# Performance work log

Measured on AMD Instinct MI355X. Metric: run time of the kernel, lower is better.

The kernel has to match this reference:

```python
import jax, jax.numpy as jnp
import numpy as np

K = 64
M = 256
V = 5000

def setup_inputs() -> dict:
    key = jax.random.key(0)
    ks = jax.random.split(key, 8)
    feat_x = jax.random.normal(ks[0], (1, V, M), dtype=jnp.float32)
    feat_y = jax.random.normal(ks[1], (1, V, M), dtype=jnp.float32)
    evals_x = jnp.sort(jax.random.uniform(ks[2], (1, K), dtype=jnp.float32))
    evals_y = jnp.sort(jax.random.uniform(ks[3], (1, K), dtype=jnp.float32))
    evecs_trans_x = jax.random.normal(ks[4], (1, K, V), dtype=jnp.float32) / np.sqrt(V)
    evecs_trans_y = jax.random.normal(ks[5], (1, K, V), dtype=jnp.float32) / np.sqrt(V)
    eye = jnp.eye(K, dtype=jnp.float32)
    sqrtMk_x = (eye + 0.05 * jax.random.normal(ks[6], (K, K), dtype=jnp.float32))[None]
    sqrtMk_y = (eye + 0.05 * jax.random.normal(ks[7], (K, K), dtype=jnp.float32))[None]
    return {"feat_x": feat_x, "feat_y": feat_y, "evals_x": evals_x, "evals_y": evals_y,
            "evecs_trans_x": evecs_trans_x, "evecs_trans_y": evecs_trans_y,
            "sqrtMk_x": sqrtMk_x, "sqrtMk_y": sqrtMk_y}

LMBDA = 0.001

def _fmap(fx, fy, ex, ey, tx, ty, sx, sy):
    # squeeze batch dim of 1 (as in torch .squeeze())
    fx, fy = fx[0], fy[0]            # [V, m]
    ex, ey = ex[0], ey[0]            # [k]
    tx, ty = tx[0], ty[0]            # [k, V]
    sx, sy = sx[0], sy[0]            # [k, k]
    A = tx @ fx                      # [k, m] spectral coeffs of feat_x
    B = sy @ (ty @ fy)               # adapt_feature=True: premultiply by sqrtMk_y
    k, m = A.shape
    vec_B = B.T.reshape(m * k, 1)
    At_Ik = jnp.kron(A.T, sy)        # [m*k, k*k] (adapt_feature -> Ik = sqrtMk_y)
    first = At_Ik.T @ At_Ik          # [k^2, k^2]
    # adapt_mask=True branch
    inv_sx = jnp.linalg.inv(sx)
    lx = jnp.diag(ex)
    ly = jnp.diag(ey)
    lx_Ik = jnp.kron(lx @ inv_sx, sy)
    Ik_ly = jnp.kron(inv_sx, sy @ ly)
    Delta = lx_Ik - Ik_ly
    second = Delta.T @ Delta
    rhs = At_Ik.T @ vec_B
    op = first + LMBDA * second
    C = jnp.linalg.solve(op, rhs)
    return C.reshape(k, k).T[None]   # [1, k, k]

def reference(feat_x, feat_y, evals_x, evals_y, evecs_trans_x, evecs_trans_y, sqrtMk_x, sqrtMk_y):
    # bidirectional=False -> only Cxy (Cyx is None in the torch module)
    return _fmap(feat_x, feat_y, evals_x, evals_y, evecs_trans_x, evecs_trans_y, sqrtMk_x, sqrtMk_y)
```

## Files before the change

### kernel.cpp

```cpp
#include <hip/hip_runtime.h>

#define LMBDA 0.001f
#define NS_SY 4
#define NS_G  5
#define NS_SX 5
#define OUTER 3
#define LDP 68

#define WS_A    0
#define WS_FY   16384
#define WS_G1   32768
#define WS_T1   36864
#define WS_R2   40960
#define WS_R4   45056
#define WS_GINV 49152
#define WS_C    53248
#define WS_FYAT 57344

#define FMA4(ar, xs, b) { ar[0]=fmaf((xs),(b).x,ar[0]); ar[1]=fmaf((xs),(b).y,ar[1]); \
                          ar[2]=fmaf((xs),(b).z,ar[2]); ar[3]=fmaf((xs),(b).w,ar[3]); }

template<int SA, int SB>
__device__ __forceinline__ void mm64(const float* __restrict__ A,
                                     const float* __restrict__ B,
                                     int ti, int tj, float a[4][4]) {
    #pragma unroll 4
    for (int k = 0; k < 64; k += 4) {
        float4 av0 = *(const float4*)&A[(4 * ti + 0) * SA + k];
        float4 av1 = *(const float4*)&A[(4 * ti + 1) * SA + k];
        float4 av2 = *(const float4*)&A[(4 * ti + 2) * SA + k];
        float4 av3 = *(const float4*)&A[(4 * ti + 3) * SA + k];
        float4 b0 = *(const float4*)&B[(k + 0) * SB + 4 * tj];
        float4 b1 = *(const float4*)&B[(k + 1) * SB + 4 * tj];
        float4 b2 = *(const float4*)&B[(k + 2) * SB + 4 * tj];
        float4 b3 = *(const float4*)&B[(k + 3) * SB + 4 * tj];
        FMA4(a[0], av0.x, b0); FMA4(a[0], av0.y, b1); FMA4(a[0], av0.z, b2); FMA4(a[0], av0.w, b3);
        FMA4(a[1], av1.x, b0); FMA4(a[1], av1.y, b1); FMA4(a[1], av1.z, b2); FMA4(a[1], av1.w, b3);
        FMA4(a[2], av2.x, b0); FMA4(a[2], av2.y, b1); FMA4(a[2], av2.z, b2); FMA4(a[2], av2.w, b3);
        FMA4(a[3], av3.x, b0); FMA4(a[3], av3.y, b1); FMA4(a[3], av3.z, b2); FMA4(a[3], av3.w, b3);
    }
}

__global__ __launch_bounds__(256) void k1_gemm(
    const float* __restrict__ tx, const float* __restrict__ fx,
    const float* __restrict__ ty, const float* __restrict__ fy,
    float* __restrict__ wsA, float* __restrict__ wsFy)
{
    __shared__ float sT[64 * LDP];
    __shared__ float sF[64 * LDP];
    const int tid = threadIdx.x;
    const int ti = tid >> 4, tj = tid & 15;
    const int mat = blockIdx.x >> 2;
    const int m0 = (blockIdx.x & 3) << 6;
    const float* __restrict__ T = mat ? ty : tx;
    const float* __restrict__ F = mat ? fy : fx;
    float* __restrict__ Out = mat ? wsFy : wsA;

    float acc[4][4];
    #pragma unroll
    for (int r = 0; r < 4; ++r)
        #pragma unroll
        for (int c = 0; c < 4; ++c) acc[r][c] = 0.f;

    for (int sc = blockIdx.y; sc * 64 < 5000; sc += 27) {
        const int v0 = sc << 6;
        int vlen = 5000 - v0; if (vlen > 64) vlen = 64;
        #pragma unroll
        for (int w = 0; w < 4; ++w) {
            const int fidx = tid + (w << 8);
            const int row = fidx >> 4, q = fidx & 15;
            const int vv = q << 2;
            if (vv < vlen) {
                float4 val = *(const float4*)(T + (size_t)row * 5000 + v0 + vv);
                sT[(vv + 0) * LDP + row] = val.x;
                sT[(vv + 1) * LDP + row] = val.y;
                sT[(vv + 2) * LDP + row] = val.z;
                sT[(vv + 3) * LDP + row] = val.w;
            }
            if (row < vlen) {
                *(float4*)&sF[row * LDP + (q << 2)] =
                    *(const float4*)(F + (size_t)(v0 + row) * 256 + m0 + (q << 2));
            }
        }
        __syncthreads();
        for (int v = 0; v < vlen; ++v) {
            float4 av = *(const float4*)&sT[v * LDP + 4 * ti];
            float4 bv = *(const float4*)&sF[v * LDP + 4 * tj];
            FMA4(acc[0], av.x, bv); FMA4(acc[1], av.y, bv);
            FMA4(acc[2], av.z, bv); FMA4(acc[3], av.w, bv);
        }
        __syncthreads();
    }
    #pragma unroll
    for (int r = 0; r < 4; ++r)
        #pragma unroll
        for (int c = 0; c < 4; ++c)
            atomicAdd(&Out[(4 * ti + r) * 256 + m0 + 4 * tj + c], acc[r][c]);
}

__device__ __forceinline__ void ns_invert(float* sM, float* sX, float* sY,
                                          int iters, int ti, int tj,
                                          int tid, float alpha)
{
    for (int idx = tid; idx < 4096; idx += 256) {
        int i = idx >> 6, j = idx & 63;
        sX[i * LDP + j] = (i == j) ? alpha : 0.f;
    }
    __syncthreads();
    for (int it = 0; it < iters; ++it) {
        float y[4][4];
        #pragma unroll
        for (int r = 0; r < 4; ++r)
            #pragma unroll
            for (int c = 0; c < 4; ++c) y[r][c] = 0.f;
        mm64<LDP, LDP>(sM, sX, ti, tj, y);
        #pragma unroll
        for (int r = 0; r < 4; ++r) {
            float4 v = {y[r][0], y[r][1], y[r][2], y[r][3]};
            *(float4*)&sY[(4 * ti + r) * 64 + 4 * tj] = v;
        }
        __syncthreads();
        float z[4][4];
        #pragma unroll
        for (int r = 0; r < 4; ++r)
            #pragma unroll
            for (int c = 0; c < 4; ++c) z[r][c] = 0.f;
        mm64<LDP, 64>(sX, sY, ti, tj, z);
        __syncthreads();
        #pragma unroll
        for (int r = 0; r < 4; ++r) {
            float4 xv = *(const float4*)&sX[(4 * ti + r) * LDP + 4 * tj];
            xv.x = 2.f * xv.x - z[r][0];
            xv.y = 2.f * xv.y - z[r][1];
            xv.z = 2.f * xv.z - z[r][2];
            xv.w = 2.f * xv.w - z[r][3];
            *(float4*)&sX[(4 * ti + r) * LDP + 4 * tj] = xv;
        }
        __syncthreads();
    }
}

__global__ __launch_bounds__(256, 1) void k2_prep(
    const float* __restrict__ wsA, const float* __restrict__ wsFy,
    const float* __restrict__ sx, const float* __restrict__ sy,
    const float* __restrict__ ex, const float* __restrict__ ey,
    float* __restrict__ ws)
{
    extern __shared__ __align__(16) float lds2[];
    const int tid = threadIdx.x;
    const int ti = tid >> 4, tj = tid & 15;
    const int b = blockIdx.x;

    if (b == 0) {
        float* sSy = lds2;
        float* sXx = lds2 + 4352;
        float* sYy = lds2 + 8704;
        float* sH  = lds2 + 12800;
        float* sV  = lds2 + 16896;
        for (int idx = tid; idx < 1024; idx += 256) {
            int i = idx >> 4, j4 = (idx & 15) << 2;
            *(float4*)&sSy[i * LDP + j4] = *(const float4*)&sy[i * 64 + j4];
        }
        if (tid < 64) sV[tid] = ey[tid];
        __syncthreads();
        {
            float h[4][4];
            #pragma unroll
            for (int r = 0; r < 4; ++r)
                #pragma unroll
                for (int c = 0; c < 4; ++c) h[r][c] = 0.f;
            for (int k = 0; k < 64; ++k) {
                float4 av = *(const float4*)&sSy[k * LDP + 4 * ti];
                float4 bv = *(const float4*)&sSy[k * LDP + 4 * tj];
                FMA4(h[0], av.x, bv); FMA4(h[1], av.y, bv);
                FMA4(h[2], av.z, bv); FMA4(h[3], av.w, bv);
            }
            #pragma unroll
            for (int r = 0; r < 4; ++r) {
                float4 v = {h[r][0], h[r][1], h[r][2], h[r][3]};
                *(float4*)&sH[(4 * ti + r) * 64 + 4 * tj] = v;
            }
        }
        __syncthreads();
        ns_invert(sSy, sXx, sYy, NS_SY, ti, tj, tid, 1.0f);
        {
            float h[4][4];
            #pragma unroll
            for (int r = 0; r < 4; ++r)
                #pragma unroll
                for (int c = 0; c < 4; ++c) h[r][c] = 0.f;
            for (int m = 0; m < 64; m += 4) {
                float4 av[4], bv[4];
                #pragma unroll
                for (int r = 0; r < 4; ++r) av[r] = *(const float4*)&sXx[(4 * ti + r) * LDP + m];
                #pragma unroll
                for (int c = 0; c < 4; ++c) bv[c] = *(const float4*)&sXx[(4 * tj + c) * LDP + m];
                #pragma unroll
                for (int r = 0; r < 4; ++r)
                    #pragma unroll
                    for (int c = 0; c < 4; ++c)
                        h[r][c] += av[r].x * bv[c].x + av[r].y * bv[c].y
                                 + av[r].z * bv[c].z + av[r].w * bv[c].w;
            }
            __syncthreads();
            #pragma unroll
            for (int r = 0; r < 4; ++r) {
                float4 v = {h[r][0], h[r][1], h[r][2], h[r][3]};
                *(float4*)&sSy[(4 * ti + r) * LDP + 4 * tj] = v;
            }
        }
        __syncthreads();
        {
            float a[4][4];
            #pragma unroll
            for (int r = 0; r < 4; ++r)
                #pragma unroll
                for (int c = 0; c < 4; ++c) a[r][c] = 0.f;
            #pragma unroll 4
            for (int k = 0; k < 64; k += 4) {
                float4 av[4];
                #pragma unroll
                for (int r = 0; r < 4; ++r) av[r] = *(const float4*)&sSy[(4 * ti + r) * LDP + k];
                #pragma unroll
                for (int q = 0; q < 4; ++q) {
                    float e = sV[k + q];
                    float4 bv = *(const float4*)&sH[(k + q) * 64 + 4 * tj];
                    bv.x *= e; bv.y *= e; bv.z *= e; bv.w *= e;
                    float xq[4] = {av[0].x, av[1].x, av[2].x, av[3].x};
                    if (q == 1) { xq[0]=av[0].y; xq[1]=av[1].y; xq[2]=av[2].y; xq[3]=av[3].y; }
                    if (q == 2) { xq[0]=av[0].z; xq[1]=av[1].z; xq[2]=av[2].z; xq[3]=av[3].z; }
                    if (q == 3) { xq[0]=av[0].w; xq[1]=av[1].w; xq[2]=av[2].w; xq[3]=av[3].w; }
                    #pragma unroll
                    for (int r = 0; r < 4; ++r) FMA4(a[r], xq[r], bv);
                }
            }
            #pragma unroll
            for (int r = 0; r < 4; ++r) {
                float4 v = {a[r][0], a[r][1], a[r][2], a[r][3]};
                *(float4*)&ws[WS_C + (4 * ti + r) * 64 + 4 * tj] = v;
            }
        }
    } else if (b == 1) {
        float* sA = lds2;
        float* sG = lds2 + 4352;
        float* sX = lds2 + 8704;
        float* sY = lds2 + 13056;
        float* sV = lds2 + 17152;
        float a[4][4];
        #pragma unroll
        for (int r = 0; r < 4; ++r)
            #pragma unroll
            for (int c = 0; c < 4; ++c) a[r][c] = 0.f;
        for (int ch = 0; ch < 4; ++ch) {
            for (int idx = tid; idx < 1024; idx += 256) {
                int i = idx >> 4, m4 = (idx & 15) << 2;
                *(float4*)&sA[i * LDP + m4] =
                    *(const float4*)&wsA[i * 256 + (ch << 6) + m4];
            }
            __syncthreads();
            for (int m = 0; m < 64; m += 4) {
                float4 av[4], bv[4];
                #pragma unroll
                for (int r = 0; r < 4; ++r) av[r] = *(const float4*)&sA[(4 * ti + r) * LDP + m];
                #pragma unroll
                for (int c = 0; c < 4; ++c) bv[c] = *(const float4*)&sA[(4 * tj + c) * LDP + m];
                #pragma unroll
                for (int r = 0; r < 4; ++r)
                    #pragma unroll
                    for (int c = 0; c < 4; ++c)
                        a[r][c] += av[r].x * bv[c].x + av[r].y * bv[c].y
                                 + av[r].z * bv[c].z + av[r].w * bv[c].w;
            }
            __syncthreads();
        }
        #pragma unroll
        for (int r = 0; r < 4; ++r) {
            float4 v = {a[r][0], a[r][1], a[r][2], a[r][3]};
            *(float4*)&sG[(4 * ti + r) * LDP + 4 * tj] = v;
            *(float4*)&ws[WS_G1 + (4 * ti + r) * 64 + 4 * tj] = v;
        }
        __syncthreads();
        if (tid < 64) {
            float s = 0.f;
            for (int j4 = 0; j4 < 64; j4 += 4) {
                float4 v = *(const float4*)&sG[tid * LDP + j4];
                s += v.x * v.x + v.y * v.y + v.z * v.z + v.w * v.w;
            }
            sV[tid] = s;
            sV[64 + tid] = sG[tid * LDP + tid];
        }
        __syncthreads();
        float f2 = 0.f, tr = 0.f;
        for (int i = 0; i < 64; ++i) { f2 += sV[i]; tr += sV[64 + i]; }
        ns_invert(sG, sX, sY, NS_G, ti, tj, tid, tr / f2);
        for (int idx = tid; idx < 1024; idx += 256) {
            int i = idx >> 4, j4 = (idx & 15) << 2;
            *(float4*)&ws[WS_GINV + i * 64 + j4] = *(const float4*)&sX[i * LDP + j4];
        }
    } else if (b == 2) {
        float* sM = lds2;
        float* sX = lds2 + 4352;
        float* sY = lds2 + 8704;
        float* sV = lds2 + 12800;
        for (int idx = tid; idx < 1024; idx += 256) {
            int i = idx >> 4, j4 = (idx & 15) << 2;
            *(float4*)&sM[i * LDP + j4] = *(const float4*)&sx[i * 64 + j4];
        }
        if (tid < 64) sV[tid] = ex[tid];
        __syncthreads();
        ns_invert(sM, sX, sY, NS_SX, ti, tj, tid, 1.0f);
        float aR2[4][4], aR4[4][4], aT1[4][4];
        #pragma unroll
        for (int r = 0; r < 4; ++r)
            #pragma unroll
            for (int c = 0; c < 4; ++c) { aR2[r][c] = 0.f; aR4[r][c] = 0.f; aT1[r][c] = 0.f; }
        for (int k = 0; k < 64; ++k) {
            float e = sV[k], e2 = e * e;
            float4 av = *(const float4*)&sX[k * LDP + 4 * ti];
            float4 bv = *(const float4*)&sX[k * LDP + 4 * tj];
            float avv[4] = {av.x, av.y, av.z, av.w};
            #pragma unroll
            for (int r = 0; r < 4; ++r) {
                FMA4(aR4[r], avv[r], bv);
                float ea = e * avv[r];
                FMA4(aR2[r], ea, bv);
                float e2a = e2 * avv[r];
                FMA4(aT1[r], e2a, bv);
            }
        }
        #pragma unroll
        for (int r = 0; r < 4; ++r) {
            int o = (4 * ti + r) * 64 + 4 * tj;
            float4 v2 = {aR2[r][0], aR2[r][1], aR2[r][2], aR2[r][3]};
            float4 v4 = {aR4[r][0], aR4[r][1], aR4[r][2], aR4[r][3]};
            float4 v1 = {aT1[r][0], aT1[r][1], aT1[r][2], aT1[r][3]};
            *(float4*)&ws[WS_R2 + o] = v2;
            *(float4*)&ws[WS_R4 + o] = v4;
            *(float4*)&ws[WS_T1 + o] = v1;
        }
    } else {
        float* sFy = lds2;
        float* sAx = lds2 + 4352;
        float a[4][4];
        #pragma unroll
        for (int r = 0; r < 4; ++r)
            #pragma unroll
            for (int c = 0; c < 4; ++c) a[r][c] = 0.f;
        for (int ch = 0; ch < 4; ++ch) {
            for (int idx = tid; idx < 1024; idx += 256) {
                int i = idx >> 4, m4 = (idx & 15) << 2;
                *(float4*)&sFy[i * LDP + m4] = *(const float4*)&wsFy[i * 256 + (ch << 6) + m4];
                *(float4*)&sAx[i * LDP + m4] = *(const float4*)&wsA[i * 256 + (ch << 6) + m4];
            }
            __syncthreads();
            for (int m = 0; m < 64; m += 4) {
                float4 av[4], bv[4];
                #pragma unroll
                for (int r = 0; r < 4; ++r) av[r] = *(const float4*)&sFy[(4 * ti + r) * LDP + m];
                #pragma unroll
                for (int c = 0; c < 4; ++c) bv[c] = *(const float4*)&sAx[(4 * tj + c) * LDP + m];
                #pragma unroll
                for (int r = 0; r < 4; ++r)
                    #pragma unroll
                    for (int c = 0; c < 4; ++c)
                        a[r][c] += av[r].x * bv[c].x + av[r].y * bv[c].y
                                 + av[r].z * bv[c].z + av[r].w * bv[c].w;
            }
            __syncthreads();
        }
        #pragma unroll
        for (int r = 0; r < 4; ++r) {
            float4 v = {a[r][0], a[r][1], a[r][2], a[r][3]};
            *(float4*)&ws[WS_FYAT + (4 * ti + r) * 64 + 4 * tj] = v;
        }
    }
}

__global__ __launch_bounds__(256, 1) void k3_solve(
    const float* __restrict__ ws, const float* __restrict__ ey_g,
    float* __restrict__ out)
{
    extern __shared__ __align__(16) float lds3[];
    float* cM1   = lds3;
    float* cR2   = lds3 + 4096;
    float* cR4   = lds3 + 8192;
    float* cGinv = lds3 + 12288;
    float* sE    = lds3 + 16384;
    float* sX    = lds3 + 20480;
    float* cC    = lds3 + 24832;
    float* sW    = lds3 + 29184;
    const int tid = threadIdx.x;
    const int ti = tid >> 4, tj = tid & 15;

    for (int idx = tid; idx < 1024; idx += 256) {
        int i = idx >> 4, j4 = (idx & 15) << 2;
        int o = i * 64 + j4;
        float4 g = *(const float4*)&ws[WS_G1 + o];
        float4 t = *(const float4*)&ws[WS_T1 + o];
        float4 m = {fmaf(LMBDA, t.x, g.x), fmaf(LMBDA, t.y, g.y),
                    fmaf(LMBDA, t.z, g.z), fmaf(LMBDA, t.w, g.w)};
        *(float4*)&cM1[o]   = m;
        *(float4*)&cR2[o]   = *(const float4*)&ws[WS_R2 + o];
        *(float4*)&cR4[o]   = *(const float4*)&ws[WS_R4 + o];
        *(float4*)&cGinv[o] = *(const float4*)&ws[WS_GINV + o];
        *(float4*)&cC[i * LDP + j4] = *(const float4*)&ws[WS_C + o];
    }
    float4 eyv = *(const float4*)&ey_g[4 * ti];
    float eyr[4] = {eyv.x, eyv.y, eyv.z, eyv.w};
    float leyr[4];
    #pragma unroll
    for (int r = 0; r < 4; ++r) leyr[r] = LMBDA * eyr[r];

    float fyr[4][4], xreg[4][4];
    #pragma unroll
    for (int r = 0; r < 4; ++r) {
        float4 v = *(const float4*)&ws[WS_FYAT + (4 * ti + r) * 64 + 4 * tj];
        fyr[r][0] = v.x; fyr[r][1] = v.y; fyr[r][2] = v.z; fyr[r][3] = v.w;
        float4 z = {0.f, 0.f, 0.f, 0.f};
        *(float4*)&sX[(4 * ti + r) * LDP + 4 * tj] = z;
        #pragma unroll
        for (int c = 0; c < 4; ++c) xreg[r][c] = 0.f;
    }
    __syncthreads();

    float E1[4][4];
    for (int it = 0; it < OUTER; ++it) {
        {
            float Sm[4][4], S2[4][4], S4[4][4];
            #pragma unroll
            for (int r = 0; r < 4; ++r)
                #pragma unroll
                for (int c = 0; c < 4; ++c) { Sm[r][c] = 0.f; S2[r][c] = 0.f; S4[r][c] = 0.f; }
            #pragma unroll 2
            for (int k = 0; k < 64; k += 4) {
                float4 av[4];
                #pragma unroll
                for (int r = 0; r < 4; ++r)
                    av[r] = *(const float4*)&sX[(4 * ti + r) * LDP + k];
                #pragma unroll
                for (int q = 0; q < 4; ++q) {
                    float4 mv = *(const float4*)&cM1[(k + q) * 64 + 4 * tj];
                    float4 qv = *(const float4*)&cR2[(k + q) * 64 + 4 * tj];
                    float4 rv = *(const float4*)&cR4[(k + q) * 64 + 4 * tj];
                    float xq[4] = {av[0].x, av[1].x, av[2].x, av[3].x};
                    if (q == 1) { xq[0]=av[0].y; xq[1]=av[1].y; xq[2]=av[2].y; xq[3]=av[3].y; }
                    if (q == 2) { xq[0]=av[0].z; xq[1]=av[1].z; xq[2]=av[2].z; xq[3]=av[3].z; }
                    if (q == 3) { xq[0]=av[0].w; xq[1]=av[1].w; xq[2]=av[2].w; xq[3]=av[3].w; }
                    #pragma unroll
                    for (int r = 0; r < 4; ++r) {
                        FMA4(Sm[r], xq[r], mv);
                        FMA4(S2[r], xq[r], qv);
                        FMA4(S4[r], xq[r], rv);
                    }
                }
            }
            #pragma unroll
            for (int r = 0; r < 4; ++r) {
                float4 e2;
                e2.x = LMBDA * fmaf(eyr[r], S4[r][0], -S2[r][0]);
                e2.y = LMBDA * fmaf(eyr[r], S4[r][1], -S2[r][1]);
                e2.z = LMBDA * fmaf(eyr[r], S4[r][2], -S2[r][2]);
                e2.w = LMBDA * fmaf(eyr[r], S4[r][3], -S2[r][3]);
                *(float4*)&sE[(4 * ti + r) * 64 + 4 * tj] = e2;
                #pragma unroll
                for (int c = 0; c < 4; ++c)
                    E1[r][c] = fmaf(-leyr[r], S2[r][c], Sm[r][c]);
            }
        }
        __syncthreads();
        {
            float Z[4][4];
            #pragma unroll
            for (int r = 0; r < 4; ++r)
                #pragma unroll
                for (int c = 0; c < 4; ++c) Z[r][c] = 0.f;
            mm64<LDP, 64>(cC, sE, ti, tj, Z);
            #pragma unroll
            for (int r = 0; r < 4; ++r) {
                float4 w;
                w.x = fyr[r][0] - E1[r][0] - Z[r][0];
                w.y = fyr[r][1] - E1[r][1] - Z[r][1];
                w.z = fyr[r][2] - E1[r][2] - Z[r][2];
                w.w = fyr[r][3] - E1[r][3] - Z[r][3];
                *(float4*)&sW[(4 * ti + r) * LDP + 4 * tj] = w;
            }
        }
        __syncthreads();
        {
            float dX[4][4];
            #pragma unroll
            for (int r = 0; r < 4; ++r)
                #pragma unroll
                for (int c = 0; c < 4; ++c) dX[r][c] = 0.f;
            mm64<LDP, 64>(sW, cGinv, ti, tj, dX);
            #pragma unroll
            for (int r = 0; r < 4; ++r) {
                float4 v;
                #pragma unroll
                for (int c = 0; c < 4; ++c) xreg[r][c] += dX[r][c];
                v.x = xreg[r][0]; v.y = xreg[r][1]; v.z = xreg[r][2]; v.w = xreg[r][3];
                *(float4*)&sX[(4 * ti + r) * LDP + 4 * tj] = v;
                if (it == OUTER - 1)
                    *(float4*)&out[(4 * ti + r) * 64 + 4 * tj] = v;
            }
        }
        if (it == OUTER - 1) break;
        __syncthreads();
    }
}

extern "C" void kernel_launch(void* const* d_in, const int* in_sizes, int n_in,
                              void* d_out, int out_size, void* d_ws, size_t ws_size,
                              hipStream_t stream) {
    (void)in_sizes; (void)n_in; (void)out_size; (void)ws_size;
    const float* fx = (const float*)d_in[0];
    const float* fy = (const float*)d_in[1];
    const float* ex = (const float*)d_in[2];
    const float* ey = (const float*)d_in[3];
    const float* tx = (const float*)d_in[4];
    const float* ty = (const float*)d_in[5];
    const float* sx = (const float*)d_in[6];
    const float* sy = (const float*)d_in[7];
    float* ws = (float*)d_ws;
    float* out = (float*)d_out;

    (void)hipFuncSetAttribute((const void*)k2_prep,
                              hipFuncAttributeMaxDynamicSharedMemorySize, 69120);
    (void)hipFuncSetAttribute((const void*)k3_solve,
                              hipFuncAttributeMaxDynamicSharedMemorySize, 134144);

    (void)hipMemsetAsync(d_ws, 0, 2 * 64 * 256 * sizeof(float), stream);
    k1_gemm<<<dim3(8, 27), 256, 0, stream>>>(tx, fx, ty, fy, ws + WS_A, ws + WS_FY);
    k2_prep<<<4, 256, 69120, stream>>>(ws + WS_A, ws + WS_FY, sx, sy, ex, ey, ws);
    k3_solve<<<1, 256, 134144, stream>>>(ws, ey, out);
}
```

Measured before the change: 181.5 us.

## Fuse prep and solve kernels with atomic-counter sync and split-K partial buffers

Merges the prep and solve kernels into one launch where helper blocks signal completion through a global atomic counter. When the workspace is large enough, the spectral GEMM writes per-split partial sums, which removes the memset and the atomics and cuts the split count. It also drops one Newton-Schulz iteration for inv(sx) and restructures some small matmuls. In exchange the design relies on blocks of one launch running concurrently (spin-wait) and accepts a slightly less converged inverse.

```diff
diff --git a/kernel.cpp b/kernel.cpp
--- a/kernel.cpp
+++ b/kernel.cpp
@@ -3,19 +3,19 @@
 #define LMBDA 0.001f
 #define NS_SY 4
 #define NS_G  5
-#define NS_SX 5
+#define NS_SX 4
 #define OUTER 3
 #define LDP 68
-
-#define WS_A    0
-#define WS_FY   16384
-#define WS_G1   32768
-#define WS_T1   36864
-#define WS_R2   40960
-#define WS_R4   45056
-#define WS_GINV 49152
-#define WS_C    53248
-#define WS_FYAT 57344
+#define SPLITS 8
+
+#define WS_R2   32768
+#define WS_R4   36864
+#define WS_T1   40960
+#define WS_C    45056
+#define WS_FYAT 49152
+#define WS_CTR  53248
+#define WS_PART 53312
+#define WS_NEED ((WS_PART + SPLITS * 32768) * 4)
 
 #define FMA4(ar, xs, b) { ar[0]=fmaf((xs),(b).x,ar[0]); ar[1]=fmaf((xs),(b).y,ar[1]); \
                           ar[2]=fmaf((xs),(b).z,ar[2]); ar[3]=fmaf((xs),(b).w,ar[3]); }
@@ -41,63 +41,6 @@
     }
 }
 
-__global__ __launch_bounds__(256) void k1_gemm(
-    const float* __restrict__ tx, const float* __restrict__ fx,
-    const float* __restrict__ ty, const float* __restrict__ fy,
-    float* __restrict__ wsA, float* __restrict__ wsFy)
-{
-    __shared__ float sT[64 * LDP];
-    __shared__ float sF[64 * LDP];
-    const int tid = threadIdx.x;
-    const int ti = tid >> 4, tj = tid & 15;
-    const int mat = blockIdx.x >> 2;
-    const int m0 = (blockIdx.x & 3) << 6;
-    const float* __restrict__ T = mat ? ty : tx;
-    const float* __restrict__ F = mat ? fy : fx;
-    float* __restrict__ Out = mat ? wsFy : wsA;
-
-    float acc[4][4];
-    #pragma unroll
-    for (int r = 0; r < 4; ++r)
-        #pragma unroll
-        for (int c = 0; c < 4; ++c) acc[r][c] = 0.f;
-
-    for (int sc = blockIdx.y; sc * 64 < 5000; sc += 27) {
-        const int v0 = sc << 6;
-        int vlen = 5000 - v0; if (vlen > 64) vlen = 64;
-        #pragma unroll
-        for (int w = 0; w < 4; ++w) {
-            const int fidx = tid + (w << 8);
-            const int row = fidx >> 4, q = fidx & 15;
-            const int vv = q << 2;
-            if (vv < vlen) {
-                float4 val = *(const float4*)(T + (size_t)row * 5000 + v0 + vv);
-                sT[(vv + 0) * LDP + row] = val.x;
-                sT[(vv + 1) * LDP + row] = val.y;
-                sT[(vv + 2) * LDP + row] = val.z;
-                sT[(vv + 3) * LDP + row] = val.w;
-            }
-            if (row < vlen) {
-                *(float4*)&sF[row * LDP + (q << 2)] =
-                    *(const float4*)(F + (size_t)(v0 + row) * 256 + m0 + (q << 2));
-            }
-        }
-        __syncthreads();
-        for (int v = 0; v < vlen; ++v) {
-            float4 av = *(const float4*)&sT[v * LDP + 4 * ti];
-            float4 bv = *(const float4*)&sF[v * LDP + 4 * tj];
-            FMA4(acc[0], av.x, bv); FMA4(acc[1], av.y, bv);
-            FMA4(acc[2], av.z, bv); FMA4(acc[3], av.w, bv);
-        }
-        __syncthreads();
-    }
-    #pragma unroll
-    for (int r = 0; r < 4; ++r)
-        #pragma unroll
-        for (int c = 0; c < 4; ++c)
-            atomicAdd(&Out[(4 * ti + r) * 256 + m0 + 4 * tj + c], acc[r][c]);
-}
-
 __device__ __forceinline__ void ns_invert(float* sM, float* sX, float* sY,
                                           int iters, int ti, int tj,
                                           int tid, float alpha)
@@ -140,26 +83,96 @@
     }
 }
 
-__global__ __launch_bounds__(256, 1) void k2_prep(
-    const float* __restrict__ wsA, const float* __restrict__ wsFy,
+__global__ __launch_bounds__(256) void k1_gemm(
+    const float* __restrict__ tx, const float* __restrict__ fx,
+    const float* __restrict__ ty, const float* __restrict__ fy,
+    float* __restrict__ ws, int nparts, int pbase)
+{
+    __shared__ float sT[64 * LDP];
+    __shared__ float sF[64 * LDP];
+    const int tid = threadIdx.x;
+    const int ti = tid >> 4, tj = tid & 15;
+    const int mat = blockIdx.x >> 2;
+    const int m0 = (blockIdx.x & 3) << 6;
+    const float* __restrict__ T = mat ? ty : tx;
+    const float* __restrict__ F = mat ? fy : fx;
+    float* __restrict__ Out = ws + pbase +
+        (nparts > 1 ? (int)blockIdx.y * 32768 : 0) + mat * 16384;
+
+    if (blockIdx.x == 0 && blockIdx.y == 0 && tid == 0)
+        ((unsigned*)(ws + WS_CTR))[0] = 0u;
+
+    float acc[4][4];
+    #pragma unroll
+    for (int r = 0; r < 4; ++r)
+        #pragma unroll
+        for (int c = 0; c < 4; ++c) acc[r][c] = 0.f;
+
+    for (int sc = blockIdx.y; sc * 64 < 5000; sc += gridDim.y) {
+        const int v0 = sc << 6;
+        int vlen = 5000 - v0; if (vlen > 64) vlen = 64;
+        #pragma unroll
+        for (int w = 0; w < 4; ++w) {
+            const int fidx = tid + (w << 8);
+            const int row = fidx >> 4, q = fidx & 15;
+            const int vv = q << 2;
+            if (vv < vlen) {
+                float4 val = *(const float4*)(T + (size_t)row * 5000 + v0 + vv);
+                sT[(vv + 0) * LDP + row] = val.x;
+                sT[(vv + 1) * LDP + row] = val.y;
+                sT[(vv + 2) * LDP + row] = val.z;
+                sT[(vv + 3) * LDP + row] = val.w;
+            }
+            if (row < vlen) {
+                *(float4*)&sF[row * LDP + (q << 2)] =
+                    *(const float4*)(F + (size_t)(v0 + row) * 256 + m0 + (q << 2));
+            }
+        }
+        __syncthreads();
+        for (int v = 0; v < vlen; ++v) {
+            float4 av = *(const float4*)&sT[v * LDP + 4 * ti];
+            float4 bv = *(const float4*)&sF[v * LDP + 4 * tj];
+            FMA4(acc[0], av.x, bv); FMA4(acc[1], av.y, bv);
+            FMA4(acc[2], av.z, bv); FMA4(acc[3], av.w, bv);
+        }
+        __syncthreads();
+    }
+    if (nparts > 1) {
+        #pragma unroll
+        for (int r = 0; r < 4; ++r) {
+            float4 v = {acc[r][0], acc[r][1], acc[r][2], acc[r][3]};
+            *(float4*)&Out[(4 * ti + r) * 256 + m0 + 4 * tj] = v;
+        }
+    } else {
+        #pragma unroll
+        for (int r = 0; r < 4; ++r)
+            #pragma unroll
+            for (int c = 0; c < 4; ++c)
+                atomicAdd(&Out[(4 * ti + r) * 256 + m0 + 4 * tj + c], acc[r][c]);
+    }
+}
+
+__global__ __launch_bounds__(256, 1) void k23_fused(
+    float* __restrict__ ws,
     const float* __restrict__ sx, const float* __restrict__ sy,
     const float* __restrict__ ex, const float* __restrict__ ey,
-    float* __restrict__ ws)
+    float* __restrict__ out, int nparts, int pbase)
 {
-    extern __shared__ __align__(16) float lds2[];
+    extern __shared__ __align__(16) float lds[];
     const int tid = threadIdx.x;
     const int ti = tid >> 4, tj = tid & 15;
     const int b = blockIdx.x;
-
-    if (b == 0) {
-        float* sSy = lds2;
-        float* sXx = lds2 + 4352;
-        float* sYy = lds2 + 8704;
-        float* sH  = lds2 + 12800;
-        float* sV  = lds2 + 16896;
+    unsigned* ctr = (unsigned*)(ws + WS_CTR);
+
+    if (b == 1) {
+        float* s0 = lds;
+        float* s1 = lds + 4352;
+        float* s2 = lds + 8704;
+        float* s3 = lds + 12800;
+        float* sV = lds + 16896;
         for (int idx = tid; idx < 1024; idx += 256) {
             int i = idx >> 4, j4 = (idx & 15) << 2;
-            *(float4*)&sSy[i * LDP + j4] = *(const float4*)&sy[i * 64 + j4];
+            *(float4*)&s0[i * LDP + j4] = *(const float4*)&sy[i * 64 + j4];
         }
         if (tid < 64) sV[tid] = ey[tid];
         __syncthreads();
@@ -170,43 +183,42 @@
                 #pragma unroll
                 for (int c = 0; c < 4; ++c) h[r][c] = 0.f;
             for (int k = 0; k < 64; ++k) {
-                float4 av = *(const float4*)&sSy[k * LDP + 4 * ti];
-                float4 bv = *(const float4*)&sSy[k * LDP + 4 * tj];
+                float4 av = *(const float4*)&s0[k * LDP + 4 * ti];
+                float4 bv = *(const float4*)&s0[k * LDP + 4 * tj];
                 FMA4(h[0], av.x, bv); FMA4(h[1], av.y, bv);
                 FMA4(h[2], av.z, bv); FMA4(h[3], av.w, bv);
             }
             #pragma unroll
             for (int r = 0; r < 4; ++r) {
                 float4 v = {h[r][0], h[r][1], h[r][2], h[r][3]};
-                *(float4*)&sH[(4 * ti + r) * 64 + 4 * tj] = v;
-            }
-        }
-        __syncthreads();
-        ns_invert(sSy, sXx, sYy, NS_SY, ti, tj, tid, 1.0f);
+                *(float4*)&s3[(4 * ti + r) * 64 + 4 * tj] = v;
+            }
+        }
+        __syncthreads();
+        ns_invert(s0, s1, s2, NS_SY, ti, tj, tid, 1.0f);
         {
-            float h[4][4];
+            float z[4][4];
             #pragma unroll
             for (int r = 0; r < 4; ++r)
                 #pragma unroll
-                for (int c = 0; c < 4; ++c) h[r][c] = 0.f;
-            for (int m = 0; m < 64; m += 4) {
-                float4 av[4], bv[4];
-                #pragma unroll
-                for (int r = 0; r < 4; ++r) av[r] = *(const float4*)&sXx[(4 * ti + r) * LDP + m];
-                #pragma unroll
-                for (int c = 0; c < 4; ++c) bv[c] = *(const float4*)&sXx[(4 * tj + c) * LDP + m];
-                #pragma unroll
-                for (int r = 0; r < 4; ++r)
-                    #pragma unroll
-                    for (int c = 0; c < 4; ++c)
-                        h[r][c] += av[r].x * bv[c].x + av[r].y * bv[c].y
-                                 + av[r].z * bv[c].z + av[r].w * bv[c].w;
+                for (int c = 0; c < 4; ++c) z[r][c] = 0.f;
+            #pragma unroll 4
+            for (int k = 0; k < 64; ++k) {
+                float e = sV[k];
+                float a0 = s1[k * LDP + 4 * ti + 0];
+                float a1 = s1[k * LDP + 4 * ti + 1];
+                float a2 = s1[k * LDP + 4 * ti + 2];
+                float a3 = s1[k * LDP + 4 * ti + 3];
+                float4 bv = *(const float4*)&s3[k * 64 + 4 * tj];
+                bv.x *= e; bv.y *= e; bv.z *= e; bv.w *= e;
+                FMA4(z[0], a0, bv); FMA4(z[1], a1, bv);
+                FMA4(z[2], a2, bv); FMA4(z[3], a3, bv);
             }
             __syncthreads();
             #pragma unroll
             for (int r = 0; r < 4; ++r) {
-                float4 v = {h[r][0], h[r][1], h[r][2], h[r][3]};
-                *(float4*)&sSy[(4 * ti + r) * LDP + 4 * tj] = v;
+                float4 v = {z[r][0], z[r][1], z[r][2], z[r][3]};
+                *(float4*)&s2[(4 * ti + r) * 64 + 4 * tj] = v;
             }
         }
         __syncthreads();
@@ -216,99 +228,28 @@
             for (int r = 0; r < 4; ++r)
                 #pragma unroll
                 for (int c = 0; c < 4; ++c) a[r][c] = 0.f;
-            #pragma unroll 4
-            for (int k = 0; k < 64; k += 4) {
-                float4 av[4];
-                #pragma unroll
-                for (int r = 0; r < 4; ++r) av[r] = *(const float4*)&sSy[(4 * ti + r) * LDP + k];
-                #pragma unroll
-                for (int q = 0; q < 4; ++q) {
-                    float e = sV[k + q];
-                    float4 bv = *(const float4*)&sH[(k + q) * 64 + 4 * tj];
-                    bv.x *= e; bv.y *= e; bv.z *= e; bv.w *= e;
-                    float xq[4] = {av[0].x, av[1].x, av[2].x, av[3].x};
-                    if (q == 1) { xq[0]=av[0].y; xq[1]=av[1].y; xq[2]=av[2].y; xq[3]=av[3].y; }
-                    if (q == 2) { xq[0]=av[0].z; xq[1]=av[1].z; xq[2]=av[2].z; xq[3]=av[3].z; }
-                    if (q == 3) { xq[0]=av[0].w; xq[1]=av[1].w; xq[2]=av[2].w; xq[3]=av[3].w; }
-                    #pragma unroll
-                    for (int r = 0; r < 4; ++r) FMA4(a[r], xq[r], bv);
-                }
-            }
+            mm64<LDP, 64>(s1, s2, ti, tj, a);
             #pragma unroll
             for (int r = 0; r < 4; ++r) {
                 float4 v = {a[r][0], a[r][1], a[r][2], a[r][3]};
                 *(float4*)&ws[WS_C + (4 * ti + r) * 64 + 4 * tj] = v;
             }
         }
-    } else if (b == 1) {
-        float* sA = lds2;
-        float* sG = lds2 + 4352;
-        float* sX = lds2 + 8704;
-        float* sY = lds2 + 13056;
-        float* sV = lds2 + 17152;
-        float a[4][4];
-        #pragma unroll
-        for (int r = 0; r < 4; ++r)
-            #pragma unroll
-            for (int c = 0; c < 4; ++c) a[r][c] = 0.f;
-        for (int ch = 0; ch < 4; ++ch) {
-            for (int idx = tid; idx < 1024; idx += 256) {
-                int i = idx >> 4, m4 = (idx & 15) << 2;
-                *(float4*)&sA[i * LDP + m4] =
-                    *(const float4*)&wsA[i * 256 + (ch << 6) + m4];
-            }
-            __syncthreads();
-            for (int m = 0; m < 64; m += 4) {
-                float4 av[4], bv[4];
-                #pragma unroll
-                for (int r = 0; r < 4; ++r) av[r] = *(const float4*)&sA[(4 * ti + r) * LDP + m];
-                #pragma unroll
-                for (int c = 0; c < 4; ++c) bv[c] = *(const float4*)&sA[(4 * tj + c) * LDP + m];
-                #pragma unroll
-                for (int r = 0; r < 4; ++r)
-                    #pragma unroll
-                    for (int c = 0; c < 4; ++c)
-                        a[r][c] += av[r].x * bv[c].x + av[r].y * bv[c].y
-                                 + av[r].z * bv[c].z + av[r].w * bv[c].w;
-            }
-            __syncthreads();
-        }
-        #pragma unroll
-        for (int r = 0; r < 4; ++r) {
-            float4 v = {a[r][0], a[r][1], a[r][2], a[r][3]};
-            *(float4*)&sG[(4 * ti + r) * LDP + 4 * tj] = v;
-            *(float4*)&ws[WS_G1 + (4 * ti + r) * 64 + 4 * tj] = v;
-        }
-        __syncthreads();
-        if (tid < 64) {
-            float s = 0.f;
-            for (int j4 = 0; j4 < 64; j4 += 4) {
-                float4 v = *(const float4*)&sG[tid * LDP + j4];
-                s += v.x * v.x + v.y * v.y + v.z * v.z + v.w * v.w;
-            }
-            sV[tid] = s;
-            sV[64 + tid] = sG[tid * LDP + tid];
-        }
-        __syncthreads();
-        float f2 = 0.f, tr = 0.f;
-        for (int i = 0; i < 64; ++i) { f2 += sV[i]; tr += sV[64 + i]; }
-        ns_invert(sG, sX, sY, NS_G, ti, tj, tid, tr / f2);
+        __threadfence();
+        __syncthreads();
+        if (tid == 0) atomicAdd(ctr, 1u);
+    } else if (b == 2) {
+        float* s0 = lds;
+        float* s1 = lds + 4352;
+        float* s2 = lds + 8704;
+        float* sV = lds + 16896;
         for (int idx = tid; idx < 1024; idx += 256) {
             int i = idx >> 4, j4 = (idx & 15) << 2;
-            *(float4*)&ws[WS_GINV + i * 64 + j4] = *(const float4*)&sX[i * LDP + j4];
-        }
-    } else if (b == 2) {
-        float* sM = lds2;
-        float* sX = lds2 + 4352;
-        float* sY = lds2 + 8704;
-        float* sV = lds2 + 12800;
-        for (int idx = tid; idx < 1024; idx += 256) {
-            int i = idx >> 4, j4 = (idx & 15) << 2;
-            *(float4*)&sM[i * LDP + j4] = *(const float4*)&sx[i * 64 + j4];
+            *(float4*)&s0[i * LDP + j4] = *(const float4*)&sx[i * 64 + j4];
         }
         if (tid < 64) sV[tid] = ex[tid];
         __syncthreads();
-        ns_invert(sM, sX, sY, NS_SX, ti, tj, tid, 1.0f);
+        ns_invert(s0, s1, s2, NS_SX, ti, tj, tid, 1.0f);
         float aR2[4][4], aR4[4][4], aT1[4][4];
         #pragma unroll
         for (int r = 0; r < 4; ++r)
@@ -316,8 +257,8 @@
             for (int c = 0; c < 4; ++c) { aR2[r][c] = 0.f; aR4[r][c] = 0.f; aT1[r][c] = 0.f; }
         for (int k = 0; k < 64; ++k) {
             float e = sV[k], e2 = e * e;
-            float4 av = *(const float4*)&sX[k * LDP + 4 * ti];
-            float4 bv = *(const float4*)&sX[k * LDP + 4 * tj];
+            float4 av = *(const float4*)&s1[k * LDP + 4 * ti];
+            float4 bv = *(const float4*)&s1[k * LDP + 4 * tj];
             float avv[4] = {av.x, av.y, av.z, av.w};
             #pragma unroll
             for (int r = 0; r < 4; ++r) {
@@ -338,9 +279,12 @@
             *(float4*)&ws[WS_R4 + o] = v4;
             *(float4*)&ws[WS_T1 + o] = v1;
         }
-    } else {
-        float* sFy = lds2;
-        float* sAx = lds2 + 4352;
+        __threadfence();
+        __syncthreads();
+        if (tid == 0) atomicAdd(ctr, 1u);
+    } else if (b == 3) {
+        float* s0 = lds;
+        float* s1 = lds + 4352;
         float a[4][4];
         #pragma unroll
         for (int r = 0; r < 4; ++r)
@@ -349,22 +293,25 @@
         for (int ch = 0; ch < 4; ++ch) {
             for (int idx = tid; idx < 1024; idx += 256) {
                 int i = idx >> 4, m4 = (idx & 15) << 2;
-                *(float4*)&sFy[i * LDP + m4] = *(const float4*)&wsFy[i * 256 + (ch << 6) + m4];
-                *(float4*)&sAx[i * LDP + m4] = *(const float4*)&wsA[i * 256 + (ch << 6) + m4];
+                float4 va = {0.f, 0.f, 0.f, 0.f}, vf = {0.f, 0.f, 0.f, 0.f};
+                for (int s = 0; s < nparts; ++s) {
+                    const float* p = ws + pbase + s * 32768;
+                    float4 x = *(const float4*)&p[i * 256 + (ch << 6) + m4];
+                    va.x += x.x; va.y += x.y; va.z += x.z; va.w += x.w;
+                    float4 y = *(const float4*)&p[16384 + i * 256 + (ch << 6) + m4];
+                    vf.x += y.x; vf.y += y.y; vf.z += y.z; vf.w += y.w;
+                }
+                s0[(m4 + 0) * LDP + i] = va.x; s0[(m4 + 1) * LDP + i] = va.y;
+                s0[(m4 + 2) * LDP + i] = va.z; s0[(m4 + 3) * LDP + i] = va.w;
+                s1[(m4 + 0) * LDP + i] = vf.x; s1[(m4 + 1) * LDP + i] = vf.y;
+                s1[(m4 + 2) * LDP + i] = vf.z; s1[(m4 + 3) * LDP + i] = vf.w;
             }
             __syncthreads();
-            for (int m = 0; m < 64; m += 4) {
-                float4 av[4], bv[4];
-                #pragma unroll
-                for (int r = 0; r < 4; ++r) av[r] = *(const float4*)&sFy[(4 * ti + r) * LDP + m];
-                #pragma unroll
-                for (int c = 0; c < 4; ++c) bv[c] = *(const float4*)&sAx[(4 * tj + c) * LDP + m];
-                #pragma unroll
-                for (int r = 0; r < 4; ++r)
-                    #pragma unroll
-                    for (int c = 0; c < 4; ++c)
-                        a[r][c] += av[r].x * bv[c].x + av[r].y * bv[c].y
-                                 + av[r].z * bv[c].z + av[r].w * bv[c].w;
+            for (int m = 0; m < 64; ++m) {
+                float4 fv = *(const float4*)&s1[m * LDP + 4 * ti];
+                float4 av = *(const float4*)&s0[m * LDP + 4 * tj];
+                FMA4(a[0], fv.x, av); FMA4(a[1], fv.y, av);
+                FMA4(a[2], fv.z, av); FMA4(a[3], fv.w, av);
             }
             __syncthreads();
         }
@@ -373,146 +320,198 @@
             float4 v = {a[r][0], a[r][1], a[r][2], a[r][3]};
             *(float4*)&ws[WS_FYAT + (4 * ti + r) * 64 + 4 * tj] = v;
         }
-    }
-}
-
-__global__ __launch_bounds__(256, 1) void k3_solve(
-    const float* __restrict__ ws, const float* __restrict__ ey_g,
-    float* __restrict__ out)
-{
-    extern __shared__ __align__(16) float lds3[];
-    float* cM1   = lds3;
-    float* cR2   = lds3 + 4096;
-    float* cR4   = lds3 + 8192;
-    float* cGinv = lds3 + 12288;
-    float* sE    = lds3 + 16384;
-    float* sX    = lds3 + 20480;
-    float* cC    = lds3 + 24832;
-    float* sW    = lds3 + 29184;
-    const int tid = threadIdx.x;
-    const int ti = tid >> 4, tj = tid & 15;
-
-    for (int idx = tid; idx < 1024; idx += 256) {
-        int i = idx >> 4, j4 = (idx & 15) << 2;
-        int o = i * 64 + j4;
-        float4 g = *(const float4*)&ws[WS_G1 + o];
-        float4 t = *(const float4*)&ws[WS_T1 + o];
-        float4 m = {fmaf(LMBDA, t.x, g.x), fmaf(LMBDA, t.y, g.y),
-                    fmaf(LMBDA, t.z, g.z), fmaf(LMBDA, t.w, g.w)};
-        *(float4*)&cM1[o]   = m;
-        *(float4*)&cR2[o]   = *(const float4*)&ws[WS_R2 + o];
-        *(float4*)&cR4[o]   = *(const float4*)&ws[WS_R4 + o];
-        *(float4*)&cGinv[o] = *(const float4*)&ws[WS_GINV + o];
-        *(float4*)&cC[i * LDP + j4] = *(const float4*)&ws[WS_C + o];
-    }
-    float4 eyv = *(const float4*)&ey_g[4 * ti];
-    float eyr[4] = {eyv.x, eyv.y, eyv.z, eyv.w};
-    float leyr[4];
-    #pragma unroll
-    for (int r = 0; r < 4; ++r) leyr[r] = LMBDA * eyr[r];
-
-    float fyr[4][4], xreg[4][4];
-    #pragma unroll
-    for (int r = 0; r < 4; ++r) {
-        float4 v = *(const float4*)&ws[WS_FYAT + (4 * ti + r) * 64 + 4 * tj];
-        fyr[r][0] = v.x; fyr[r][1] = v.y; fyr[r][2] = v.z; fyr[r][3] = v.w;
-        float4 z = {0.f, 0.f, 0.f, 0.f};
-        *(float4*)&sX[(4 * ti + r) * LDP + 4 * tj] = z;
-        #pragma unroll
-        for (int c = 0; c < 4; ++c) xreg[r][c] = 0.f;
-    }
-    __syncthreads();
-
-    float E1[4][4];
-    for (int it = 0; it < OUTER; ++it) {
+        __threadfence();
+        __syncthreads();
+        if (tid == 0) atomicAdd(ctr, 1u);
+    } else {
+        float* cM1   = lds;
+        float* cR2   = lds + 4096;
+        float* cR4   = lds + 8192;
+        float* cGinv = lds + 12288;
+        float* sE    = lds + 16384;
+        float* sX    = lds + 20480;
+        float* cC    = lds + 24832;
+        float* sW    = lds + 29184;
+        float* sV    = lds + 33536;
+        float* sAT = cC;
+        float* sG  = sW;
+        float* sXx = sX;
+        float* sYy = sE;
         {
-            float Sm[4][4], S2[4][4], S4[4][4];
+            float a[4][4];
             #pragma unroll
             for (int r = 0; r < 4; ++r)
                 #pragma unroll
-                for (int c = 0; c < 4; ++c) { Sm[r][c] = 0.f; S2[r][c] = 0.f; S4[r][c] = 0.f; }
-            #pragma unroll 2
-            for (int k = 0; k < 64; k += 4) {
-                float4 av[4];
+                for (int c = 0; c < 4; ++c) a[r][c] = 0.f;
+            for (int ch = 0; ch < 4; ++ch) {
+                for (int idx = tid; idx < 1024; idx += 256) {
+                    int i = idx >> 4, m4 = (idx & 15) << 2;
+                    float4 va = {0.f, 0.f, 0.f, 0.f};
+                    for (int s = 0; s < nparts; ++s) {
+                        float4 x = *(const float4*)&ws[pbase + s * 32768 + i * 256 + (ch << 6) + m4];
+                        va.x += x.x; va.y += x.y; va.z += x.z; va.w += x.w;
+                    }
+                    sAT[(m4 + 0) * LDP + i] = va.x; sAT[(m4 + 1) * LDP + i] = va.y;
+                    sAT[(m4 + 2) * LDP + i] = va.z; sAT[(m4 + 3) * LDP + i] = va.w;
+                }
+                __syncthreads();
+                for (int m = 0; m < 64; ++m) {
+                    float4 av = *(const float4*)&sAT[m * LDP + 4 * ti];
+                    float4 bv = *(const float4*)&sAT[m * LDP + 4 * tj];
+                    FMA4(a[0], av.x, bv); FMA4(a[1], av.y, bv);
+                    FMA4(a[2], av.z, bv); FMA4(a[3], av.w, bv);
+                }
+                __syncthreads();
+            }
+            #pragma unroll
+            for (int r = 0; r < 4; ++r) {
+                float4 v = {a[r][0], a[r][1], a[r][2], a[r][3]};
+                *(float4*)&sG[(4 * ti + r) * LDP + 4 * tj] = v;
+            }
+        }
+        __syncthreads();
+        if (tid < 64) {
+            float s = 0.f;
+            for (int j4 = 0; j4 < 64; j4 += 4) {
+                float4 v = *(const float4*)&sG[tid * LDP + j4];
+                s += v.x * v.x + v.y * v.y + v.z * v.z + v.w * v.w;
+            }
+            sV[tid] = s;
+            sV[64 + tid] = sG[tid * LDP + tid];
+        }
+        __syncthreads();
+        float f2 = 0.f, tr = 0.f;
+        for (int i = 0; i < 64; ++i) { f2 += sV[i]; tr += sV[64 + i]; }
+        ns_invert(sG, sXx, sYy, NS_G, ti, tj, tid, tr / f2);
+        if (tid == 0) {
+            while (atomicAdd(ctr, 0u) < 3u) {}
+            __threadfence();
+        }
+        __syncthreads();
+        for (int idx = tid; idx < 1024; idx += 256) {
+            int i = idx >> 4, j4 = (idx & 15) << 2;
+            int o = i * 64 + j4;
+            *(float4*)&cGinv[o] = *(const float4*)&sXx[i * LDP + j4];
+            float4 g = *(const float4*)&sG[i * LDP + j4];
+            float4 t = *(const float4*)&ws[WS_T1 + o];
+            float4 m = {fmaf(LMBDA, t.x, g.x), fmaf(LMBDA, t.y, g.y),
+                        fmaf(LMBDA, t.z, g.z), fmaf(LMBDA, t.w, g.w)};
+            *(float4*)&cM1[o] = m;
+            *(float4*)&cR2[o] = *(const float4*)&ws[WS_R2 + o];
+            *(float4*)&cR4[o] = *(const float4*)&ws[WS_R4 + o];
+        }
+        __syncthreads();
+        for (int idx = tid; idx < 1024; idx += 256) {
+            int i = idx >> 4, j4 = (idx & 15) << 2;
+            *(float4*)&cC[i * LDP + j4] = *(const float4*)&ws[WS_C + i * 64 + j4];
+            float4 z = {0.f, 0.f, 0.f, 0.f};
+            *(float4*)&sX[i * LDP + j4] = z;
+        }
+        float4 eyv = *(const float4*)&ey[4 * ti];
+        float eyr[4] = {eyv.x, eyv.y, eyv.z, eyv.w};
+        float leyr[4];
+        #pragma unroll
+        for (int r = 0; r < 4; ++r) leyr[r] = LMBDA * eyr[r];
+        float fyr[4][4], xreg[4][4], E1[4][4];
+        #pragma unroll
+        for (int r = 0; r < 4; ++r) {
+            float4 v = *(const float4*)&ws[WS_FYAT + (4 * ti + r) * 64 + 4 * tj];
+            fyr[r][0] = v.x; fyr[r][1] = v.y; fyr[r][2] = v.z; fyr[r][3] = v.w;
+            #pragma unroll
+            for (int c = 0; c < 4; ++c) xreg[r][c] = 0.f;
+        }
+        __syncthreads();
+
+        for (int it = 0; it < OUTER; ++it) {
+            {
+                float Sm[4][4], S2[4][4], S4[4][4];
                 #pragma unroll
                 for (int r = 0; r < 4; ++r)
-                    av[r] = *(const float4*)&sX[(4 * ti + r) * LDP + k];
-                #pragma unroll
-                for (int q = 0; q < 4; ++q) {
-                    float4 mv = *(const float4*)&cM1[(k + q) * 64 + 4 * tj];
-                    float4 qv = *(const float4*)&cR2[(k + q) * 64 + 4 * tj];
-                    float4 rv = *(const float4*)&cR4[(k + q) * 64 + 4 * tj];
-                    float xq[4] = {av[0].x, av[1].x, av[2].x, av[3].x};
-                    if (q == 1) { xq[0]=av[0].y; xq[1]=av[1].y; xq[2]=av[2].y; xq[3]=av[3].y; }
-                    if (q == 2) { xq[0]=av[0].z; xq[1]=av[1].z; xq[2]=av[2].z; xq[3]=av[3].z; }
-                    if (q == 3) { xq[0]=av[0].w; xq[1]=av[1].w; xq[2]=av[2].w; xq[3]=av[3].w; }
-                    #pragma unroll
-                    for (int r = 0; r < 4; ++r) {
-                        FMA4(Sm[r], xq[r], mv);
-                        FMA4(S2[r], xq[r], qv);
-                        FMA4(S4[r], xq[r], rv);
+                    #pragma unroll
+                    for (int c = 0; c < 4; ++c) { Sm[r][c] = 0.f; S2[r][c] = 0.f; S4[r][c] = 0.f; }
+                #pragma unroll 2
+                for (int k = 0; k < 64; k += 4) {
+                    float4 av[4];
+                    #pragma unroll
+                    for (int r = 0; r < 4; ++r)
+                        av[r] = *(const float4*)&sX[(4 * ti + r) * LDP + k];
+                    #pragma unroll
+                    for (int q = 0; q < 4; ++q) {
+                        float4 mv = *(const float4*)&cM1[(k + q) * 64 + 4 * tj];
+                        float4 qv = *(const float4*)&cR2[(k + q) * 64 + 4 * tj];
+                        float4 rv = *(const float4*)&cR4[(k + q) * 64 + 4 * tj];
+                        float xq[4] = {av[0].x, av[1].x, av[2].x, av[3].x};
+                        if (q == 1) { xq[0]=av[0].y; xq[1]=av[1].y; xq[2]=av[2].y; xq[3]=av[3].y; }
+                        if (q == 2) { xq[0]=av[0].z; xq[1]=av[1].z; xq[2]=av[2].z; xq[3]=av[3].z; }
+                        if (q == 3) { xq[0]=av[0].w; xq[1]=av[1].w; xq[2]=av[2].w; xq[3]=av[3].w; }
+                        #pragma unroll
+                        for (int r = 0; r < 4; ++r) {
+                            FMA4(Sm[r], xq[r], mv);
+                            FMA4(S2[r], xq[r], qv);
+                            FMA4(S4[r], xq[r], rv);
+                        }
                     }
                 }
-            }
-            #pragma unroll
-            for (int r = 0; r < 4; ++r) {
-                float4 e2;
-                e2.x = LMBDA * fmaf(eyr[r], S4[r][0], -S2[r][0]);
-                e2.y = LMBDA * fmaf(eyr[r], S4[r][1], -S2[r][1]);
-                e2.z = LMBDA * fmaf(eyr[r], S4[r][2], -S2[r][2]);
-                e2.w = LMBDA * fmaf(eyr[r], S4[r][3], -S2[r][3]);
-                *(float4*)&sE[(4 * ti + r) * 64 + 4 * tj] = e2;
-                #pragma unroll
-                for (int c = 0; c < 4; ++c)
-                    E1[r][c] = fmaf(-leyr[r], S2[r][c], Sm[r][c]);
-            }
-        }
-        __syncthreads();
-        {
-            float Z[4][4];
-            #pragma unroll
-            for (int r = 0; r < 4; ++r)
-                #pragma unroll
-                for (int c = 0; c < 4; ++c) Z[r][c] = 0.f;
-            mm64<LDP, 64>(cC, sE, ti, tj, Z);
-            #pragma unroll
-            for (int r = 0; r < 4; ++r) {
-                float4 w;
-                w.x = fyr[r][0] - E1[r][0] - Z[r][0];
-                w.y = fyr[r][1] - E1[r][1] - Z[r][1];
-                w.z = fyr[r][2] - E1[r][2] - Z[r][2];
-                w.w = fyr[r][3] - E1[r][3] - Z[r][3];
-                *(float4*)&sW[(4 * ti + r) * LDP + 4 * tj] = w;
-            }
-        }
-        __syncthreads();
-        {
-            float dX[4][4];
-            #pragma unroll
-            for (int r = 0; r < 4; ++r)
-                #pragma unroll
-                for (int c = 0; c < 4; ++c) dX[r][c] = 0.f;
-            mm64<LDP, 64>(sW, cGinv, ti, tj, dX);
-            #pragma unroll
-            for (int r = 0; r < 4; ++r) {
-                float4 v;
-                #pragma unroll
-                for (int c = 0; c < 4; ++c) xreg[r][c] += dX[r][c];
-                v.x = xreg[r][0]; v.y = xreg[r][1]; v.z = xreg[r][2]; v.w = xreg[r][3];
-                *(float4*)&sX[(4 * ti + r) * LDP + 4 * tj] = v;
-                if (it == OUTER - 1)
-                    *(float4*)&out[(4 * ti + r) * 64 + 4 * tj] = v;
-            }
-        }
-        if (it == OUTER - 1) break;
-        __syncthreads();
+                #pragma unroll
+                for (int r = 0; r < 4; ++r) {
+                    float4 e2;
+                    e2.x = LMBDA * fmaf(eyr[r], S4[r][0], -S2[r][0]);
+                    e2.y = LMBDA * fmaf(eyr[r], S4[r][1], -S2[r][1]);
+                    e2.z = LMBDA * fmaf(eyr[r], S4[r][2], -S2[r][2]);
+                    e2.w = LMBDA * fmaf(eyr[r], S4[r][3], -S2[r][3]);
+                    *(float4*)&sE[(4 * ti + r) * 64 + 4 * tj] = e2;
+                    #pragma unroll
+                    for (int c = 0; c < 4; ++c)
+                        E1[r][c] = fmaf(-leyr[r], S2[r][c], Sm[r][c]);
+                }
+            }
+            __syncthreads();
+            {
+                float Z[4][4];
+                #pragma unroll
+                for (int r = 0; r < 4; ++r)
+                    #pragma unroll
+                    for (int c = 0; c < 4; ++c) Z[r][c] = 0.f;
+                mm64<LDP, 64>(cC, sE, ti, tj, Z);
+                #pragma unroll
+                for (int r = 0; r < 4; ++r) {
+                    float4 w;
+                    w.x = fyr[r][0] - E1[r][0] - Z[r][0];
+                    w.y = fyr[r][1] - E1[r][1] - Z[r][1];
+                    w.z = fyr[r][2] - E1[r][2] - Z[r][2];
+                    w.w = fyr[r][3] - E1[r][3] - Z[r][3];
+                    *(float4*)&sW[(4 * ti + r) * LDP + 4 * tj] = w;
+                }
+            }
+            __syncthreads();
+            {
+                float dX[4][4];
+                #pragma unroll
+                for (int r = 0; r < 4; ++r)
+                    #pragma unroll
+                    for (int c = 0; c < 4; ++c) dX[r][c] = 0.f;
+                mm64<LDP, 64>(sW, cGinv, ti, tj, dX);
+                #pragma unroll
+                for (int r = 0; r < 4; ++r) {
+                    float4 v;
+                    #pragma unroll
+                    for (int c = 0; c < 4; ++c) xreg[r][c] += dX[r][c];
+                    v.x = xreg[r][0]; v.y = xreg[r][1]; v.z = xreg[r][2]; v.w = xreg[r][3];
+                    *(float4*)&sX[(4 * ti + r) * LDP + 4 * tj] = v;
+                    if (it == OUTER - 1)
+                        *(float4*)&out[(4 * ti + r) * 64 + 4 * tj] = v;
+                }
+            }
+            if (it == OUTER - 1) break;
+            __syncthreads();
+        }
     }
 }
 
 extern "C" void kernel_launch(void* const* d_in, const int* in_sizes, int n_in,
                               void* d_out, int out_size, void* d_ws, size_t ws_size,
                               hipStream_t stream) {
-    (void)in_sizes; (void)n_in; (void)out_size; (void)ws_size;
+    (void)in_sizes; (void)n_in; (void)out_size;
     const float* fx = (const float*)d_in[0];
     const float* fy = (const float*)d_in[1];
     const float* ex = (const float*)d_in[2];
@@ -524,13 +523,16 @@
     float* ws = (float*)d_ws;
     float* out = (float*)d_out;
 
-    (void)hipFuncSetAttribute((const void*)k2_prep,
-                              hipFuncAttributeMaxDynamicSharedMemorySize, 69120);
-    (void)hipFuncSetAttribute((const void*)k3_solve,
-                              hipFuncAttributeMaxDynamicSharedMemorySize, 134144);
-
-    (void)hipMemsetAsync(d_ws, 0, 2 * 64 * 256 * sizeof(float), stream);
-    k1_gemm<<<dim3(8, 27), 256, 0, stream>>>(tx, fx, ty, fy, ws + WS_A, ws + WS_FY);
-    k2_prep<<<4, 256, 69120, stream>>>(ws + WS_A, ws + WS_FY, sx, sy, ex, ey, ws);
-    k3_solve<<<1, 256, 134144, stream>>>(ws, ey, out);
+    const bool partial = ws_size >= (size_t)WS_NEED;
+    const int nparts = partial ? SPLITS : 1;
+    const int pbase = partial ? WS_PART : 0;
+
+    (void)hipFuncSetAttribute((const void*)k23_fused,
+                              hipFuncAttributeMaxDynamicSharedMemorySize, 134656);
+
+    if (!partial)
+        (void)hipMemsetAsync(d_ws, 0, 2 * 64 * 256 * sizeof(float), stream);
+    k1_gemm<<<dim3(8, partial ? SPLITS : 27), 256, 0, stream>>>(
+        tx, fx, ty, fy, ws, nparts, pbase);
+    k23_fused<<<4, 256, 134656, stream>>>(ws, sx, sy, ex, ey, out, nparts, pbase);
 }
```

After: 234.1 us. 29.0% more time.
